# Performance work log

Measured on AMD Instinct MI355X. Metric: run time of the kernel, lower is better.

Reference implementation:

```python
import jax, jax.numpy as jnp
import numpy as np

B, S, E, H, V, NCAT = 64, 100, 256, 256, 100000, 18


def _lstm_layer(x, Wih, Whh, bih, bhh):
    # x: [S, B, in], Wih: [4H, in], Whh: [4H, H]; PyTorch gate order i,f,g,o
    h0 = jnp.zeros((x.shape[1], Whh.shape[1]), x.dtype)

    def step(carry, xt):
        h, c = carry
        g = xt @ Wih.T + h @ Whh.T + bih + bhh
        i, f, gg, o = jnp.split(g, 4, axis=-1)
        c = jax.nn.sigmoid(f) * c + jax.nn.sigmoid(i) * jnp.tanh(gg)
        h = jax.nn.sigmoid(o) * jnp.tanh(c)
        return (h, c), h

    _, ys = jax.lax.scan(step, (h0, h0), x)
    return ys


def _lstm2_last(x, p):
    # x: [B, S, E]; p: 8-tuple of layer0/layer1 weights. Returns h at last step of top layer.
    x = jnp.swapaxes(x, 0, 1)  # [S, B, E]
    y = _lstm_layer(x, p[0], p[1], p[2], p[3])
    y = _lstm_layer(y, p[4], p[5], p[6], p[7])
    return y[-1]  # [B, H]


def setup_inputs() -> dict:
    key = jax.random.key(0)
    ks = jax.random.split(key, 24)
    sc = 0.05
    def n(k, shape):
        return jax.random.normal(k, shape, dtype=jnp.float32) * sc
    inp = {
        'input_vu': jax.random.randint(ks[0], (B, S), 0, V),
        'input_vo': jax.random.randint(ks[1], (B, S), 0, V),
        'label_ro': jax.random.uniform(ks[2], (B, NCAT), dtype=jnp.float32),
        'video_embeddings': n(ks[4], (V, E)),
    }
    u = jax.random.uniform(ks[3], (B, NCAT), dtype=jnp.float32) + 1e-3
    inp['label_ru'] = u / u.sum(-1, keepdims=True)  # valid prob dist (KL target)
    # lstm_vu params (2 layers)
    inp['vu_Wih0'] = n(ks[5], (4 * H, E)); inp['vu_Whh0'] = n(ks[6], (4 * H, H))
    inp['vu_bih0'] = n(ks[7], (4 * H,));  inp['vu_bhh0'] = n(ks[8], (4 * H,))
    inp['vu_Wih1'] = n(ks[9], (4 * H, H)); inp['vu_Whh1'] = n(ks[10], (4 * H, H))
    inp['vu_bih1'] = n(ks[11], (4 * H,)); inp['vu_bhh1'] = n(ks[12], (4 * H,))
    # lstm_vo params
    inp['vo_Wih0'] = n(ks[13], (4 * H, E)); inp['vo_Whh0'] = n(ks[14], (4 * H, H))
    inp['vo_bih0'] = n(ks[15], (4 * H,)); inp['vo_bhh0'] = n(ks[16], (4 * H,))
    inp['vo_Wih1'] = n(ks[17], (4 * H, H)); inp['vo_Whh1'] = n(ks[18], (4 * H, H))
    inp['vo_bih1'] = n(ks[19], (4 * H,)); inp['vo_bhh1'] = n(ks[20], (4 * H,))
    # linears
    inp['ro_W'] = n(ks[21], (H, NCAT)); inp['ro_b'] = jnp.zeros((H,), jnp.float32)
    inp['ru_W'] = n(ks[22], (NCAT, 3 * H)); inp['ru_b'] = jnp.zeros((NCAT,), jnp.float32)
    return inp


def reference(input_vu, input_vo, label_ro, label_ru, video_embeddings,
              vu_Wih0, vu_Whh0, vu_bih0, vu_bhh0, vu_Wih1, vu_Whh1, vu_bih1, vu_bhh1,
              vo_Wih0, vo_Whh0, vo_bih0, vo_bhh0, vo_Wih1, vo_Whh1, vo_bih1, vo_bhh1,
              ro_W, ro_b, ru_W, ru_b):
    emb_vu = video_embeddings[input_vu]  # [B,S,E] gather
    emb_vo = video_embeddings[input_vo]
    h_vu = _lstm2_last(emb_vu, (vu_Wih0, vu_Whh0, vu_bih0, vu_bhh0,
                                vu_Wih1, vu_Whh1, vu_bih1, vu_bhh1))
    h_vo = _lstm2_last(emb_vo, (vo_Wih0, vo_Whh0, vo_bih0, vo_bhh0,
                                vo_Wih1, vo_Whh1, vo_bih1, vo_bhh1))
    enc_ro = jax.nn.relu(label_ro @ ro_W.T + ro_b)
    dec = jnp.concatenate([h_vu, h_vo, enc_ro], axis=-1) @ ru_W.T + ru_b  # [B,18]
    logp = jax.nn.log_softmax(dec, axis=-1)
    neg_logits = -(label_ru * logp).sum(-1)  # [B]
    pred = jax.nn.softmax(dec, axis=-1)
    # fused batched KL: mean_i sum_j p_ij * log2(p_ij / q_ij)
    avg_kl = (label_ru * jnp.log2(label_ru / pred)).sum(-1).mean()
    return (neg_logits, avg_kl)
```

## Files before the change

kernel.cpp:

```cpp
#include <hip/hip_runtime.h>
#include <math.h>

#define S_LEN 100
#define NCAT  18
#define HS    516
#define WSTR  520
#define FLG_OFF  262144
#define GFLG_OFF 263168
#define G_OFF    524288

typedef __attribute__((ext_vector_type(8)))  short  short8;
typedef __attribute__((ext_vector_type(16))) float  floatx16;

#define AT_LOADU(p)   __hip_atomic_load((p), __ATOMIC_RELAXED, __HIP_MEMORY_SCOPE_AGENT)
#define AT_STORE(p,v) __hip_atomic_store((p),(v), __ATOMIC_RELAXED, __HIP_MEMORY_SCOPE_AGENT)


struct Params {
  const int* ivu; const int* ivo;
  const float* lro; const float* lru;
  const float* VE;
  const float* W[4][2];
  const float* b0[4]; const float* b1[4];
  const float* roW; const float* rob;
  const float* ruW; const float* rub;
  float* ws; float* out;
};

__device__ __forceinline__ unsigned short f2bf(float f) {
  unsigned u = __builtin_bit_cast(unsigned, f);
  u += 0x7FFFu + ((u >> 16) & 1u);
  return (unsigned short)(u >> 16);
}
__device__ __forceinline__ float bf2f(unsigned short h) {
  unsigned u = ((unsigned)h) << 16;
  return __builtin_bit_cast(float, u);
}
__device__ __forceinline__ unsigned long long packbf4(float4 v) {
  return (unsigned long long)f2bf(v.x)
       | ((unsigned long long)f2bf(v.y) << 16)
       | ((unsigned long long)f2bf(v.z) << 32)
       | ((unsigned long long)f2bf(v.w) << 48);
}
__device__ __forceinline__ float sigm(float x) {
  return __builtin_amdgcn_rcpf(1.f + __expf(-x));
}
__device__ __forceinline__ float tanh_f(float x) {
  return 1.f - 2.f * __builtin_amdgcn_rcpf(1.f + __expf(2.f * x));
}

__device__ __forceinline__ floatx16 load_gtile(const char* wsb, int idx, int tid) {
  const unsigned long long* gp =
      (const unsigned long long*)(wsb + G_OFF + (size_t)idx * 16384) + tid * 8;
  floatx16 g;
  #pragma unroll
  for (int j = 0; j < 8; ++j) {
    union { unsigned long long u; float f[2]; } cv;
    cv.u = AT_LOADU(gp + j);
    g[2 * j] = cv.f[0]; g[2 * j + 1] = cv.f[1];
  }
  return g;
}

__device__ __forceinline__ void gate0_body(const Params& P, int idx) {
  char* wsb = (char*)P.ws;
  const int t = idx >> 5;
  const int r = idx & 31;
  const int inst = r >> 4, wg = r & 15;
  const int blk = (inst * 100 + t) * 16 + wg;

  const int tid = threadIdx.x, lane = tid & 63, wave = tid >> 6;
  const int jt = wave >> 1, bt = wave & 1, half = lane >> 5;
  const int trow = lane & 31;
  const int R = (trow & 3) * 256 + wg * 16 + jt * 8 + (trow >> 2);
  const int b = bt * 32 + trow;
  const int* __restrict__ idxp = inst ? P.ivo : P.ivu;
  const float* __restrict__ wih = P.W[inst][0] + (size_t)R * 256;
  const float* __restrict__ vr = P.VE + (size_t)idxp[b * S_LEN + t] * 256;

  floatx16 acc;
  #pragma unroll
  for (int rr = 0; rr < 16; ++rr) {
    const int Rr = (rr & 3) * 256 + wg * 16 + jt * 8 + 2 * (rr >> 2) + half;
    acc[rr] = P.b0[inst][Rr] + P.b1[inst][Rr];
  }
  #pragma unroll
  for (int s = 0; s < 16; ++s) {
    float4 a0 = *(const float4*)(wih + s * 16 + half * 8);
    float4 a1 = *(const float4*)(wih + s * 16 + half * 8 + 4);
    float4 e0 = *(const float4*)(vr + s * 16 + half * 8);
    float4 e1 = *(const float4*)(vr + s * 16 + half * 8 + 4);
    union { unsigned long long q[2]; short8 v; } ua, ub;
    ua.q[0] = packbf4(a0); ua.q[1] = packbf4(a1);
    ub.q[0] = packbf4(e0); ub.q[1] = packbf4(e1);
    acc = __builtin_amdgcn_mfma_f32_32x32x16_bf16(ua.v, ub.v, acc, 0, 0, 0);
  }
  unsigned long long* gd =
      (unsigned long long*)(wsb + G_OFF + (size_t)blk * 16384) + tid * 8;
  #pragma unroll
  for (int j = 0; j < 8; ++j) {
    union { float f[2]; unsigned long long u; } cv;
    cv.f[0] = acc[2 * j]; cv.f[1] = acc[2 * j + 1];
    AT_STORE(gd + j, cv.u);
  }
  __syncthreads();
  if (tid == 0) AT_STORE((unsigned*)(wsb + GFLG_OFF) + blk, 1u);
}

__global__ __launch_bounds__(256, 1) void lstm_all(Params P) {
  __shared__ short          Wlds[64 * WSTR];
  __shared__ unsigned short hstage[64 * HS];

  if (blockIdx.x >= 64) { gate0_body(P, (int)blockIdx.x - 64); return; }

  const int tid  = threadIdx.x;
  const int lane = tid & 63;
  const int wave = tid >> 6;
  const int rbk  = blockIdx.x;
  const int xcd  = rbk & 7, grpi = rbk >> 3;
  const int lstm = xcd >> 2;
  const int idx32 = grpi * 4 + (xcd & 3);
  const int layer = idx32 >> 4;
  const int wg    = idx32 & 15;
  const int inst  = layer * 2 + lstm;
  const int gb    = idx32;

  char* wsb = (char*)P.ws;
  unsigned* arr = (unsigned*)(wsb + FLG_OFF) + lstm * 128;

  const int jt = wave >> 1, bt = wave & 1;
  const int half = lane >> 5;
  const int trow = lane & 31;
  const int bl   = bt * 32 + trow;

  {
    const int jrow = tid >> 2;
    const int q    = tid & 3;
    const int tr   = jrow & 31, jts = jrow >> 5;
    const int R    = (tr & 3) * 256 + wg * 16 + jts * 8 + (tr >> 2);
    const float* wih = P.W[inst][0] + (size_t)R * 256;
    const float* whh = P.W[inst][1] + (size_t)R * 256;
    short* dst = &Wlds[jrow * WSTR];
    if (layer || q < 2) {
      #pragma unroll
      for (int k = q * 128; k < q * 128 + 128; k += 8) {
        const float* src = layer ? ((k < 256) ? (wih + k) : (whh + (k - 256)))
                                 : (whh + k);
        float4 v0 = *(const float4*)src;
        float4 v1 = *(const float4*)(src + 4);
        *(unsigned long long*)(dst + k)     = packbf4(v0);
        *(unsigned long long*)(dst + k + 4) = packbf4(v1);
      }
    }
  }
  float bias16[16];
  if (layer) {
    #pragma unroll
    for (int r = 0; r < 16; ++r) {
      const int Rr = (r & 3) * 256 + wg * 16 + jt * 8 + 2 * (r >> 2) + half;
      bias16[r] = P.b0[inst][Rr] + P.b1[inst][Rr];
    }
  }

  #pragma unroll
  for (int j = 0; j < 2; ++j) {
    const int gi = gb * 512 + tid * 2 + j;
    const int r = gi >> 12, off = gi & 4095;
    char* base = wsb + ((r < 2) ? (size_t)(lstm * 2 + r) * 32768
                                : 131072 + (size_t)(lstm * 2 + r - 2) * 32768);
    AT_STORE((unsigned long long*)base + off, 0ull);
  }
  __syncthreads();
  if (tid == 0) AT_STORE(arr + gb * 4, 1u);

  const int arow_off = (jt * 32 + trow) * WSTR + half * 8;
  const int brow_off = bl * HS + half * 8;
  const unsigned* __restrict__ gflags = (const unsigned*)(wsb + GFLG_OFF);

  floatx16 gcur;
  if (layer == 0) {
    const int gidx = (lstm * 100) * 16 + wg;
    while (AT_LOADU(gflags + gidx) == 0) { }
    gcur = load_gtile(wsb, gidx, tid);
  }
  float c[4] = {0.f, 0.f, 0.f, 0.f};

  for (int t = 0; t <= S_LEN; ++t) {
    if (wave == 0) {
      const unsigned want = (unsigned)(t + 1);
      const unsigned* slot = arr + trow * 4;
      while (!__all(AT_LOADU(slot) >= want)) { }
    }
    __syncthreads();

    const bool active = (layer == 0) ? (t < S_LEN) : (t >= 1);
    if (active) {
      const int cur = t & 1, prv = (t + 1) & 1;

      if (layer == 0) {
        const unsigned long long* s64 =
            (const unsigned long long*)(wsb + (size_t)(lstm * 2 + prv) * 32768);
        unsigned long long v[16];
        #pragma unroll
        for (int j = 0; j < 16; ++j) v[j] = AT_LOADU(s64 + tid + j * 256);
        #pragma unroll
        for (int j = 0; j < 16; ++j) {
          const int i = tid + j * 256, bb = i >> 6, kq = i & 63;
          *(unsigned long long*)&hstage[bb * HS + kq * 4] = v[j];
        }
      } else {
        const unsigned long long* lo =
            (const unsigned long long*)(wsb + (size_t)(lstm * 2 + prv) * 32768);
        const unsigned long long* hi =
            (const unsigned long long*)(wsb + 131072 + (size_t)(lstm * 2 + cur) * 32768);
        unsigned long long v[32];
        #pragma unroll
        for (int j = 0; j < 16; ++j) v[j]      = AT_LOADU(lo + tid + j * 256);
        #pragma unroll
        for (int j = 0; j < 16; ++j) v[16 + j] = AT_LOADU(hi + tid + j * 256);
        #pragma unroll
        for (int j = 0; j < 16; ++j) {
          const int i = tid + j * 256, bb = i >> 6, kq = i & 63;
          *(unsigned long long*)&hstage[bb * HS + kq * 4] = v[j];
        }
        #pragma unroll
        for (int j = 0; j < 16; ++j) {
          const int i = tid + j * 256, bb = i >> 6, kq = i & 63;
          *(unsigned long long*)&hstage[bb * HS + 256 + kq * 4] = v[16 + j];
        }
      }
      __syncthreads();

      floatx16 acc, acc2;
      if (layer == 0) {
        acc = gcur;
        #pragma unroll
        for (int r = 0; r < 16; ++r) acc2[r] = 0.f;
        #pragma unroll
        for (int s = 0; s < 16; s += 2) {
          short8 a0 = *(const short8*)&Wlds[arow_off + s * 16];
          short8 b0 = *(const short8*)&hstage[brow_off + s * 16];
          short8 a1 = *(const short8*)&Wlds[arow_off + (s + 1) * 16];
          short8 b1 = *(const short8*)&hstage[brow_off + (s + 1) * 16];
          acc  = __builtin_amdgcn_mfma_f32_32x32x16_bf16(a0, b0, acc,  0, 0, 0);
          acc2 = __builtin_amdgcn_mfma_f32_32x32x16_bf16(a1, b1, acc2, 0, 0, 0);
        }
      } else {
        #pragma unroll
        for (int r = 0; r < 16; ++r) { acc[r] = bias16[r]; acc2[r] = 0.f; }
        #pragma unroll
        for (int s = 0; s < 32; s += 2) {
          short8 a0 = *(const short8*)&Wlds[arow_off + s * 16];
          short8 b0 = *(const short8*)&hstage[brow_off + s * 16];
          short8 a1 = *(const short8*)&Wlds[arow_off + (s + 1) * 16];
          short8 b1 = *(const short8*)&hstage[brow_off + (s + 1) * 16];
          acc  = __builtin_amdgcn_mfma_f32_32x32x16_bf16(a0, b0, acc,  0, 0, 0);
          acc2 = __builtin_amdgcn_mfma_f32_32x32x16_bf16(a1, b1, acc2, 0, 0, 0);
        }
      }
      #pragma unroll
      for (int r = 0; r < 16; ++r) acc[r] += acc2[r];

      unsigned long long own = 0ull;
      #pragma unroll
      for (int q = 0; q < 4; ++q) {
        const float ig = sigm(acc[4 * q + 0]);
        const float fg = sigm(acc[4 * q + 1]);
        const float gg = tanh_f(acc[4 * q + 2]);
        const float og = sigm(acc[4 * q + 3]);
        const float cc = fg * c[q] + ig * gg;
        c[q] = cc;
        own |= ((unsigned long long)f2bf(og * tanh_f(cc))) << (16 * q);
      }
      {
        const unsigned long long oth =
            (unsigned long long)__shfl_xor((long long)own, 32, 64);
        const unsigned long long A = half ? oth : own;
        const unsigned long long B = half ? own : oth;
        const unsigned a32 = half ? (unsigned)(A >> 32) : (unsigned)A;
        const unsigned b32 = half ? (unsigned)(B >> 32) : (unsigned)B;
        const unsigned long long pack =
              (unsigned long long)(a32 & 0xFFFFu)
            | ((unsigned long long)(b32 & 0xFFFFu) << 16)
            | ((unsigned long long)(a32 >> 16) << 32)
            | ((unsigned long long)(b32 >> 16) << 48);
        unsigned long long* hout = (layer == 0)
            ? (unsigned long long*)(wsb + (size_t)(lstm * 2 + cur) * 32768)
            : (unsigned long long*)(wsb + 131072 + (size_t)(lstm * 2 + prv) * 32768);
        AT_STORE(hout + bl * 64 + wg * 4 + jt * 2 + half, pack);
      }
    }
    if (t < S_LEN) {
      __syncthreads();
      if (tid == 0) AT_STORE(arr + gb * 4, (unsigned)(t + 2));
    }
    if (layer == 0 && t + 1 < S_LEN) {
      const int gidx = (lstm * 100 + t + 1) * 16 + wg;
      while (AT_LOADU(gflags + gidx) == 0) { }
      gcur = load_gtile(wsb, gidx, tid);
    }
  }
}

__global__ __launch_bounds__(64) void head_kernel(Params P) {
  __shared__ float enc[256];
  __shared__ float dec[NCAT];
  const int b = blockIdx.x, t = threadIdx.x;
  char* wsb = (char*)P.ws;
  const unsigned short* hvu = (const unsigned short*)(wsb + 131072 + 1 * 32768) + b * 256;
  const unsigned short* hvo = (const unsigned short*)(wsb + 131072 + 3 * 32768) + b * 256;

  for (int m = t; m < 256; m += 64) {
    float s = P.rob[m];
    for (int j = 0; j < NCAT; ++j) s = fmaf(P.lro[b * NCAT + j], P.roW[m * NCAT + j], s);
    enc[m] = fmaxf(s, 0.f);
  }
  __syncthreads();
  for (int n = 0; n < NCAT; ++n) {
    const float* __restrict__ wr = P.ruW + n * 768;
    float s = 0.f;
    for (int k = t; k < 256; k += 64) {
      s = fmaf(bf2f(hvu[k]), wr[k], s);
      s = fmaf(bf2f(hvo[k]), wr[256 + k], s);
      s = fmaf(enc[k],       wr[512 + k], s);
    }
    for (int off = 32; off; off >>= 1) s += __shfl_down(s, off, 64);
    if (t == 0) dec[n] = s + P.rub[n];
  }
  __syncthreads();
  if (t == 0) {
    float M = dec[0];
    for (int j = 1; j < NCAT; ++j) M = fmaxf(M, dec[j]);
    float Ssum = 0.f;
    for (int j = 0; j < NCAT; ++j) Ssum += expf(dec[j] - M);
    const float lse = M + logf(Ssum);
    float neg = 0.f, kl = 0.f;
    for (int j = 0; j < NCAT; ++j) {
      const float lp = dec[j] - lse;
      const float q  = P.lru[b * NCAT + j];
      neg -= q * lp;
      kl  += q * (logf(q) - lp);
    }
    P.out[b] = neg;
    atomicAdd(&P.out[64], kl * 1.4426950408889634f * (1.f / 64.f));
  }
}

extern "C" void kernel_launch(void* const* d_in, const int* in_sizes, int n_in,
                              void* d_out, int out_size, void* d_ws, size_t ws_size,
                              hipStream_t stream) {
  Params P;
  P.ivu = (const int*)d_in[0];
  P.ivo = (const int*)d_in[1];
  P.lro = (const float*)d_in[2];
  if (in_sizes[3] >= in_sizes[4]) { P.VE = (const float*)d_in[3]; P.lru = (const float*)d_in[4]; }
  else                            { P.VE = (const float*)d_in[4]; P.lru = (const float*)d_in[3]; }
  P.W[0][0] = (const float*)d_in[5];  P.W[0][1] = (const float*)d_in[6];
  P.b0[0]   = (const float*)d_in[7];  P.b1[0]   = (const float*)d_in[8];
  P.W[2][0] = (const float*)d_in[9];  P.W[2][1] = (const float*)d_in[10];
  P.b0[2]   = (const float*)d_in[11]; P.b1[2]   = (const float*)d_in[12];
  P.W[1][0] = (const float*)d_in[13]; P.W[1][1] = (const float*)d_in[14];
  P.b0[1]   = (const float*)d_in[15]; P.b1[1]   = (const float*)d_in[16];
  P.W[3][0] = (const float*)d_in[17]; P.W[3][1] = (const float*)d_in[18];
  P.b0[3]   = (const float*)d_in[19]; P.b1[3]   = (const float*)d_in[20];
  P.roW = (const float*)d_in[21]; P.rob = (const float*)d_in[22];
  P.ruW = (const float*)d_in[23]; P.rub = (const float*)d_in[24];
  P.ws  = (float*)d_ws;
  P.out = (float*)d_out;

  hipMemsetAsync((char*)d_ws + FLG_OFF, 0, 16384, stream);
  hipMemsetAsync((char*)d_out + 64 * sizeof(float), 0, sizeof(float), stream);

  lstm_all<<<dim3(3264), dim3(256), 0, stream>>>(P);
  head_kernel<<<dim3(64), dim3(64), 0, stream>>>(P);
}
```

Baseline: 635.8 us.

## Fuse head into persistent LSTM kernel, store layer-0 gate tiles as bf16

The separate head kernel is removed. Each of the 64 persistent LSTM blocks now publishes a completion flag, waits until all layer-1 blocks have finished, and computes the head (linear layers, log-softmax, KL) for one batch row. The precomputed layer-0 input-gate tiles are written and read as bf16 instead of fp32, which halves that traffic. Gate-block indices are also remapped so work spreads across XCDs. The risks are a global spin-wait barrier, extra LDS use, and reduced precision in the gate preactivations.

```diff
diff --git a/kernel.cpp b/kernel.cpp
--- a/kernel.cpp
+++ b/kernel.cpp
@@ -51,22 +51,28 @@
 
 __device__ __forceinline__ floatx16 load_gtile(const char* wsb, int idx, int tid) {
   const unsigned long long* gp =
-      (const unsigned long long*)(wsb + G_OFF + (size_t)idx * 16384) + tid * 8;
+      (const unsigned long long*)(wsb + G_OFF + (size_t)idx * 8192) + tid * 4;
   floatx16 g;
   #pragma unroll
-  for (int j = 0; j < 8; ++j) {
-    union { unsigned long long u; float f[2]; } cv;
-    cv.u = AT_LOADU(gp + j);
-    g[2 * j] = cv.f[0]; g[2 * j + 1] = cv.f[1];
+  for (int j = 0; j < 4; ++j) {
+    const unsigned long long u = AT_LOADU(gp + j);
+    g[4 * j]     = bf2f((unsigned short)u);
+    g[4 * j + 1] = bf2f((unsigned short)(u >> 16));
+    g[4 * j + 2] = bf2f((unsigned short)(u >> 32));
+    g[4 * j + 3] = bf2f((unsigned short)(u >> 48));
   }
   return g;
 }
 
-__device__ __forceinline__ void gate0_body(const Params& P, int idx) {
+__device__ __forceinline__ void gate0_body(const Params& P, int k) {
   char* wsb = (char*)P.ws;
-  const int t = idx >> 5;
-  const int r = idx & 31;
-  const int inst = r >> 4, wg = r & 15;
+  const int xcd = k & 7;
+  const int r0  = k >> 3;
+  const int wg  = r0 & 15;
+  const int m   = r0 >> 4;
+  const int p   = xcd + 8 * m;
+  const int t   = p >> 1;
+  const int inst = p & 1;
   const int blk = (inst * 100 + t) * 16 + wg;
 
   const int tid = threadIdx.x, lane = tid & 63, wave = tid >> 6;
@@ -96,12 +102,13 @@
     acc = __builtin_amdgcn_mfma_f32_32x32x16_bf16(ua.v, ub.v, acc, 0, 0, 0);
   }
   unsigned long long* gd =
-      (unsigned long long*)(wsb + G_OFF + (size_t)blk * 16384) + tid * 8;
+      (unsigned long long*)(wsb + G_OFF + (size_t)blk * 8192) + tid * 4;
   #pragma unroll
-  for (int j = 0; j < 8; ++j) {
-    union { float f[2]; unsigned long long u; } cv;
-    cv.f[0] = acc[2 * j]; cv.f[1] = acc[2 * j + 1];
-    AT_STORE(gd + j, cv.u);
+  for (int j = 0; j < 4; ++j) {
+    float4 v;
+    v.x = acc[4 * j]; v.y = acc[4 * j + 1];
+    v.z = acc[4 * j + 2]; v.w = acc[4 * j + 3];
+    AT_STORE(gd + j, packbf4(v));
   }
   __syncthreads();
   if (tid == 0) AT_STORE((unsigned*)(wsb + GFLG_OFF) + blk, 1u);
@@ -110,6 +117,9 @@
 __global__ __launch_bounds__(256, 1) void lstm_all(Params P) {
   __shared__ short          Wlds[64 * WSTR];
   __shared__ unsigned short hstage[64 * HS];
+  __shared__ float          enc[256];
+  __shared__ float          hbuf[512];
+  __shared__ float          dec[NCAT];
 
   if (blockIdx.x >= 64) { gate0_body(P, (int)blockIdx.x - 64); return; }
 
@@ -300,49 +310,69 @@
       gcur = load_gtile(wsb, gidx, tid);
     }
   }
-}
-
-__global__ __launch_bounds__(64) void head_kernel(Params P) {
-  __shared__ float enc[256];
-  __shared__ float dec[NCAT];
-  const int b = blockIdx.x, t = threadIdx.x;
-  char* wsb = (char*)P.ws;
-  const unsigned short* hvu = (const unsigned short*)(wsb + 131072 + 1 * 32768) + b * 256;
-  const unsigned short* hvo = (const unsigned short*)(wsb + 131072 + 3 * 32768) + b * 256;
-
-  for (int m = t; m < 256; m += 64) {
-    float s = P.rob[m];
-    for (int j = 0; j < NCAT; ++j) s = fmaf(P.lro[b * NCAT + j], P.roW[m * NCAT + j], s);
-    enc[m] = fmaxf(s, 0.f);
-  }
+
   __syncthreads();
-  for (int n = 0; n < NCAT; ++n) {
-    const float* __restrict__ wr = P.ruW + n * 768;
-    float s = 0.f;
-    for (int k = t; k < 256; k += 64) {
-      s = fmaf(bf2f(hvu[k]), wr[k], s);
-      s = fmaf(bf2f(hvo[k]), wr[256 + k], s);
-      s = fmaf(enc[k],       wr[512 + k], s);
-    }
-    for (int off = 32; off; off >>= 1) s += __shfl_down(s, off, 64);
-    if (t == 0) dec[n] = s + P.rub[n];
+  if (tid == 0) AT_STORE(arr + gb * 4, 102u);
+  if (wave == 0) {
+    const unsigned* fb = (const unsigned*)(wsb + FLG_OFF);
+    const unsigned* slot = (trow < 16) ? (fb + (16 + trow) * 4)
+                                       : (fb + 128 + (trow) * 4);
+    while (!__all(AT_LOADU(slot) >= 102u)) { }
   }
   __syncthreads();
-  if (t == 0) {
-    float M = dec[0];
-    for (int j = 1; j < NCAT; ++j) M = fmaxf(M, dec[j]);
-    float Ssum = 0.f;
-    for (int j = 0; j < NCAT; ++j) Ssum += expf(dec[j] - M);
-    const float lse = M + logf(Ssum);
-    float neg = 0.f, kl = 0.f;
-    for (int j = 0; j < NCAT; ++j) {
-      const float lp = dec[j] - lse;
-      const float q  = P.lru[b * NCAT + j];
-      neg -= q * lp;
-      kl  += q * (logf(q) - lp);
-    }
-    P.out[b] = neg;
-    atomicAdd(&P.out[64], kl * 1.4426950408889634f * (1.f / 64.f));
+
+  {
+    const int bb = rbk;
+    {
+      float s = P.rob[tid];
+      #pragma unroll
+      for (int j2 = 0; j2 < NCAT; ++j2)
+        s = fmaf(P.lro[bb * NCAT + j2], P.roW[tid * NCAT + j2], s);
+      enc[tid] = fmaxf(s, 0.f);
+    }
+    if (tid < 128) {
+      const unsigned long long* hp = (tid < 64)
+          ? ((const unsigned long long*)(wsb + 131072 + 1 * 32768) + bb * 64)
+          : ((const unsigned long long*)(wsb + 131072 + 3 * 32768) + bb * 64);
+      const unsigned long long hv = AT_LOADU(hp + (tid & 63));
+      float* dst = &hbuf[(tid < 64 ? 0 : 256) + (tid & 63) * 4];
+      dst[0] = bf2f((unsigned short)hv);
+      dst[1] = bf2f((unsigned short)(hv >> 16));
+      dst[2] = bf2f((unsigned short)(hv >> 32));
+      dst[3] = bf2f((unsigned short)(hv >> 48));
+    }
+    __syncthreads();
+    for (int n = wave; n < NCAT; n += 4) {
+      const float* __restrict__ wr = P.ruW + n * 768;
+      float s = 0.f;
+      #pragma unroll
+      for (int jj = 0; jj < 4; ++jj) {
+        const int k = lane + 64 * jj;
+        s = fmaf(hbuf[k],       wr[k],       s);
+        s = fmaf(hbuf[256 + k], wr[256 + k], s);
+        s = fmaf(enc[k],        wr[512 + k], s);
+      }
+      #pragma unroll
+      for (int off = 32; off; off >>= 1) s += __shfl_down(s, off, 64);
+      if (lane == 0) dec[n] = s + P.rub[n];
+    }
+    __syncthreads();
+    if (tid == 0) {
+      float M = dec[0];
+      for (int j2 = 1; j2 < NCAT; ++j2) M = fmaxf(M, dec[j2]);
+      float Ssum = 0.f;
+      for (int j2 = 0; j2 < NCAT; ++j2) Ssum += expf(dec[j2] - M);
+      const float lse = M + logf(Ssum);
+      float neg = 0.f, kl = 0.f;
+      for (int j2 = 0; j2 < NCAT; ++j2) {
+        const float lp = dec[j2] - lse;
+        const float q  = P.lru[bb * NCAT + j2];
+        neg -= q * lp;
+        kl  += q * (logf(q) - lp);
+      }
+      P.out[bb] = neg;
+      atomicAdd(&P.out[64], kl * 1.4426950408889634f * (1.f / 64.f));
+    }
   }
 }
 
@@ -372,5 +402,4 @@
   hipMemsetAsync((char*)d_out + 64 * sizeof(float), 0, sizeof(float), stream);
 
   lstm_all<<<dim3(3264), dim3(256), 0, stream>>>(P);
-  head_kernel<<<dim3(64), dim3(64), 0, stream>>>(P);
-}
+}
```

After: 606.3 us. -4.6%, faster.
